# Optimization experiments

Measured on AMD Instinct MI355X. Metric: run time of the kernel, lower is better.

## Reference

```python
import jax, jax.numpy as jnp
import numpy as np

ALPHA = 0.2  # LeakyReLU negative slope
NEG_INF = -9e15


def _xavier(key, shape, gain=1.414):
    fan_in, fan_out = shape[-2], shape[-1]
    lim = gain * np.sqrt(6.0 / (fan_in + fan_out))
    return jax.random.uniform(key, shape, jnp.float32, -lim, lim)


def setup_inputs() -> dict:
    key = jax.random.key(0)
    ks = jax.random.split(key, 8)
    B, N, Din, H, Dh, Do = 8, 1024, 256, 4, 128, 64
    x = jax.random.normal(ks[0], (B, N, Din), jnp.float32)
    adj = jax.random.randint(ks[1], (B, N, N), 0, 2).astype(jnp.int32)
    W_heads = _xavier(ks[2], (H, Din, Dh))                 # per-head W
    a_heads = _xavier(ks[3], (H, 2 * Dh, 1))[..., 0]       # per-head a, [H, 2*Dh]
    W_out = _xavier(ks[4], (H * Dh, Do))                   # out_att W
    a_out = _xavier(ks[5], (2 * Do, 1))[..., 0]            # out_att a, [2*Do]
    Wf = _xavier(ks[6], (Do, Do), gain=1.0)                # fc_out linear
    bf = jnp.zeros((Do,), jnp.float32)
    return {"x": x, "adj": adj, "W_heads": W_heads, "a_heads": a_heads,
            "W_out": W_out, "a_out": a_out, "Wf": Wf, "bf": bf}


def _leaky_relu(v):
    return jnp.where(v >= 0, v, ALPHA * v)


def _gat(h, adj, W, a):
    # h: [B,N,Fin], adj: [B,N,N], W: [Fin,Fout], a: [2*Fout]
    Wh = h @ W                                   # [B,N,F]
    F = W.shape[-1]
    # additive attention: e_ij = leakyrelu(a_src.Wh_i + a_dst.Wh_j)
    src = Wh @ a[:F]                             # [B,N]
    dst = Wh @ a[F:]                             # [B,N]
    e = _leaky_relu(src[:, :, None] + dst[:, None, :])   # [B,N,N]
    scores = jnp.where(adj > 0, e, NEG_INF)
    attn = jax.nn.softmax(scores, axis=-1)       # dropout is a no-op in eval
    return attn @ Wh                             # [B,N,F]


def reference(x, adj, W_heads, a_heads, W_out, a_out, Wf, bf):
    B, N, _ = x.shape
    H, _, Dh = W_heads.shape
    # multi-head GAT, heads vmapped over leading axis of W_heads / a_heads
    heads = jax.vmap(_gat, in_axes=(None, None, 0, 0))(x, adj, W_heads, a_heads)  # [H,B,N,Dh]
    xcat = jnp.moveaxis(heads, 0, 2).reshape(B, N, H * Dh)   # concat heads, dim=2
    out = jax.nn.elu(_gat(xcat, adj, W_out, a_out))           # [B,N,Do]
    out = jax.nn.relu(out @ Wf + bf)                          # fc_out (dropout no-op)
    return out
```

## Files before the change

### kernel.cpp

```cpp
#include <hip/hip_runtime.h>
#include <hip/hip_bf16.h>

#define BSZ 8
#define NN 1024
#define DIN 256
#define NH 4
#define DH 128
#define DOUT 64
#define RTOT (BSZ*NN)
#define FCAT (NH*DH)
#define ALPHA 0.2f
#define XBLK 1024

typedef unsigned short ushortT;
typedef __attribute__((ext_vector_type(8))) short bf16x8;
typedef __attribute__((ext_vector_type(4))) float f32x4;

static __device__ __forceinline__ ushortT f2bf(float f) {
    __hip_bfloat16 h = __float2bfloat16(f);
    return *reinterpret_cast<ushortT*>(&h);
}
static __device__ __forceinline__ float bfu2f(ushortT u) {
    return __uint_as_float(((unsigned)u) << 16);
}
static __device__ __forceinline__ void split2(float v, ushortT& hi, ushortT& lo) {
    hi = f2bf(v);
    lo = f2bf(v - bfu2f(hi));
}
static __device__ __forceinline__ void gload16(const ushortT* g, ushortT* l) {
    __builtin_amdgcn_global_load_lds(
        (const __attribute__((address_space(1))) unsigned int*)(const void*)g,
        (__attribute__((address_space(3))) unsigned int*)(void*)l, 16, 0, 0);
}

__global__ __launch_bounds__(256) void k_prepw(const float* __restrict__ x,
                                               const float* __restrict__ W,
                                               const float* __restrict__ Wout,
                                               ushortT* __restrict__ xbh, ushortT* __restrict__ xbl,
                                               ushortT* __restrict__ WbTh, ushortT* __restrict__ WbTl,
                                               ushortT* __restrict__ WoTh, ushortT* __restrict__ WoTl) {
    const int bx = blockIdx.x;
    if (bx < XBLK) {
        const int g = bx * 256 + threadIdx.x;
        const float4* p = (const float4*)x + (size_t)g * 2;
        union { ushortT u[8]; uint4 q; } th, tl;
#pragma unroll
        for (int e4 = 0; e4 < 2; ++e4) {
            const float4 v = p[e4];
            split2(v.x, th.u[e4 * 4 + 0], tl.u[e4 * 4 + 0]);
            split2(v.y, th.u[e4 * 4 + 1], tl.u[e4 * 4 + 1]);
            split2(v.z, th.u[e4 * 4 + 2], tl.u[e4 * 4 + 2]);
            split2(v.w, th.u[e4 * 4 + 3], tl.u[e4 * 4 + 3]);
        }
        ((uint4*)xbh)[g] = th.q;
        ((uint4*)xbl)[g] = tl.q;
        return;
    }
    const int g2 = (bx - XBLK) * 256 + threadIdx.x;
    if (g2 < NH * DH * DIN) {
        const int h = g2 >> 15, f = (g2 >> 8) & 127, k = g2 & 255;
        const int kt = k >> 6, k64 = k & 63;
        const float v = W[(size_t)h * DIN * DH + (size_t)k * DH + f];
        ushortT hi, lo; split2(v, hi, lo);
        const int idx = ((h * 4 + kt) * 128 + f) * 64 + k64;
        WbTh[idx] = hi; WbTl[idx] = lo;
    } else {
        const int g3 = g2 - NH * DH * DIN;
        const int f = g3 >> 9, k = g3 & 511;
        const float v = Wout[(size_t)k * DOUT + f];
        ushortT hi, lo; split2(v, hi, lo);
        WoTh[g3] = hi; WoTl[g3] = lo;
    }
}

__global__ __launch_bounds__(512) void k_main(const ushortT* __restrict__ xbh,
                                              const ushortT* __restrict__ xbl,
                                              const float* __restrict__ ah_,
                                              const ushortT* __restrict__ WbTh,
                                              const ushortT* __restrict__ WbTl,
                                              const int* __restrict__ adj,
                                              unsigned* __restrict__ adjbit,
                                              ushortT* __restrict__ WhT,
                                              float* __restrict__ src1,
                                              float* __restrict__ dst1) {
    __shared__ ushortT Ah[128 * 64], Al[128 * 64];
    __shared__ ushortT Bh[128 * 64], Bl[128 * 64];
    __shared__ float sred[8][32], dred[8][32];
    const int tid = threadIdx.x;
    if (blockIdx.x >= 256) {
        const int g = (blockIdx.x - 256) * 512 + tid;
        const int row = g >> 5, w = g & 31;
        const int4* p = (const int4*)(adj + (size_t)row * NN + w * 32);
        unsigned m = 0;
#pragma unroll
        for (int q = 0; q < 8; ++q) {
            const int4 v = p[q];
            m |= (v.x > 0 ? 1u : 0u) << (q * 4 + 0);
            m |= (v.y > 0 ? 1u : 0u) << (q * 4 + 1);
            m |= (v.z > 0 ? 1u : 0u) << (q * 4 + 2);
            m |= (v.w > 0 ? 1u : 0u) << (q * 4 + 3);
        }
        adjbit[g] = m;
        return;
    }
    const int lane = tid & 63, wave = tid >> 6;
    const int h = blockIdx.x >> 6, mt = blockIdx.x & 63;
    const int r0 = mt * 128, b = r0 >> 10, jr = r0 & 1023;
    const int m16 = lane & 15, quad = lane >> 4;
    const int mg = wave >> 1, fg = wave & 1;
    f32x4 acc[2][4];
#pragma unroll
    for (int a = 0; a < 2; ++a)
#pragma unroll
        for (int c = 0; c < 4; ++c) acc[a][c] = (f32x4){0.f, 0.f, 0.f, 0.f};

    for (int kt = 0; kt < 4; ++kt) {
        __syncthreads();
        const ushortT* planeH = WbTh + (size_t)((h * 4 + kt) * 128) * 64;
        const ushortT* planeL = WbTl + (size_t)((h * 4 + kt) * 128) * 64;
#pragma unroll
        for (int half = 0; half < 2; ++half) {
            const int f = wave * 16 + half * 8 + (lane >> 3);
            const int sc = (lane & 7) ^ (f & 7);
            gload16(planeH + (size_t)f * 64 + sc * 8, Bh + (wave * 16 + half * 8) * 64);
            gload16(planeL + (size_t)f * 64 + sc * 8, Bl + (wave * 16 + half * 8) * 64);
        }
#pragma unroll
        for (int half = 0; half < 2; ++half) {
            const int r = wave * 16 + half * 8 + (lane >> 3);
            const int sc = (lane & 7) ^ (r & 7);
            gload16(xbh + (size_t)(r0 + r) * DIN + kt * 64 + sc * 8, Ah + (wave * 16 + half * 8) * 64);
            gload16(xbl + (size_t)(r0 + r) * DIN + kt * 64 + sc * 8, Al + (wave * 16 + half * 8) * 64);
        }
        __syncthreads();
#pragma unroll
        for (int ks = 0; ks < 2; ++ks) {
            bf16x8 a_h[2], a_l[2], b_h[4], b_l[4];
#pragma unroll
            for (int ms = 0; ms < 2; ++ms) {
                const int row = (mg * 2 + ms) * 16 + m16;
                const int cl = (ks * 4 + quad) ^ (row & 7);
                a_h[ms] = *(const bf16x8*)&Ah[row * 64 + cl * 8];
                a_l[ms] = *(const bf16x8*)&Al[row * 64 + cl * 8];
            }
#pragma unroll
            for (int fs = 0; fs < 4; ++fs) {
                const int row = (fg * 4 + fs) * 16 + m16;
                const int cl = (ks * 4 + quad) ^ (row & 7);
                b_h[fs] = *(const bf16x8*)&Bh[row * 64 + cl * 8];
                b_l[fs] = *(const bf16x8*)&Bl[row * 64 + cl * 8];
            }
#pragma unroll
            for (int ms = 0; ms < 2; ++ms)
#pragma unroll
                for (int fs = 0; fs < 4; ++fs) {
                    acc[ms][fs] = __builtin_amdgcn_mfma_f32_16x16x32_bf16(a_h[ms], b_h[fs], acc[ms][fs], 0, 0, 0);
                    acc[ms][fs] = __builtin_amdgcn_mfma_f32_16x16x32_bf16(a_h[ms], b_l[fs], acc[ms][fs], 0, 0, 0);
                    acc[ms][fs] = __builtin_amdgcn_mfma_f32_16x16x32_bf16(a_l[ms], b_h[fs], acc[ms][fs], 0, 0, 0);
                }
        }
    }
    float sacc[2][4] = {{0,0,0,0},{0,0,0,0}}, dacc[2][4] = {{0,0,0,0},{0,0,0,0}};
#pragma unroll
    for (int ms = 0; ms < 2; ++ms)
#pragma unroll
        for (int fs = 0; fs < 4; ++fs) {
            const int fl = (fg * 4 + fs) * 16 + m16;
            const float a_s = ah_[h * 2 * DH + fl];
            const float a_d = ah_[h * 2 * DH + DH + fl];
            union { ushortT u[4]; uint2 q; } tw;
#pragma unroll
            for (int reg = 0; reg < 4; ++reg) {
                const float v = acc[ms][fs][reg];
                sacc[ms][reg] += v * a_s;
                dacc[ms][reg] += v * a_d;
                tw.u[reg] = f2bf(v);
            }
            *(uint2*)(WhT + ((size_t)((b * NH + h) * DH + fl)) * NN + jr + (mg * 2 + ms) * 16 + quad * 4) = tw.q;
        }
#pragma unroll
    for (int ms = 0; ms < 2; ++ms) {
#pragma unroll
        for (int reg = 0; reg < 4; ++reg) {
            float s = sacc[ms][reg], d = dacc[ms][reg];
#pragma unroll
            for (int o = 8; o > 0; o >>= 1) {
                s += __shfl_xor(s, o, 64);
                d += __shfl_xor(d, o, 64);
            }
            if (m16 == 0) {
                sred[wave][ms * 16 + quad * 4 + reg] = s;
                dred[wave][ms * 16 + quad * 4 + reg] = d;
            }
        }
    }
    __syncthreads();
    if (tid < 128) {
        const int mgr = tid >> 5, idx = tid & 31;
        src1[h * RTOT + r0 + tid] = sred[mgr * 2][idx] + sred[mgr * 2 + 1][idx];
        dst1[h * RTOT + r0 + tid] = dred[mgr * 2][idx] + dred[mgr * 2 + 1][idx];
    }
}

__global__ __launch_bounds__(512, 2) void k_attn1(const unsigned* __restrict__ adjbit,
                                                  const ushortT* __restrict__ WhT,
                                                  const float* __restrict__ src1,
                                                  const float* __restrict__ dst1,
                                                  ushortT* __restrict__ xcat) {
    __shared__ ushortT Bs[2][128 * 64];
    __shared__ unsigned maskS[128 * 34];
    __shared__ float dstv[NN];
    __shared__ float rowinv[128], red8[8];
    const int tid = threadIdx.x, lane = tid & 63, wave = tid >> 6;
    const int bh = blockIdx.x & 31, it = blockIdx.x >> 5;
    const int b = bh >> 2, h = bh & 3;
    const int i0 = it * 128;
    const int m16 = lane & 15, quad = lane >> 4;
    const ushortT* Bbase = WhT + (size_t)(bh * DH) * NN;

#define STAGEB(kt_, buf_)                                                                  \
    {                                                                                      \
        _Pragma("unroll")                                                                  \
        for (int half = 0; half < 2; ++half) {                                             \
            const int f = wave * 16 + half * 8 + (lane >> 3);                              \
            gload16(Bbase + (size_t)f * NN + (kt_) * 64 + (((lane & 7) ^ (f & 7)) * 8),    \
                    &Bs[(buf_)][(wave * 16 + half * 8) * 64]);                             \
        }                                                                                  \
    }

    STAGEB(0, 0);
    {
        const uint4* msrc = (const uint4*)(adjbit + (size_t)(b * NN + i0) * 32) + tid * 2;
        const uint4 w0 = msrc[0], w1 = msrc[1];
        unsigned* mdst = &maskS[(tid >> 2) * 34 + (tid & 3) * 8];
        *(uint2*)&mdst[0] = make_uint2(w0.x, w0.y);
        *(uint2*)&mdst[2] = make_uint2(w0.z, w0.w);
        *(uint2*)&mdst[4] = make_uint2(w1.x, w1.y);
        *(uint2*)&mdst[6] = make_uint2(w1.z, w1.w);
    }
    float lm = -INFINITY;
#pragma unroll
    for (int k2 = 0; k2 < 2; ++k2) {
        const float d = dst1[h * RTOT + b * NN + tid + 512 * k2];
        dstv[tid + 512 * k2] = d;
        lm = fmaxf(lm, d);
    }
    const float si = src1[h * RTOT + b * NN + i0 + wave * 16 + m16];
#pragma unroll
    for (int o = 32; o > 0; o >>= 1) lm = fmaxf(lm, __shfl_xor(lm, o, 64));
    if (lane == 0) red8[wave] = lm;
    __syncthreads();
    float dmax = red8[0];
#pragma unroll
    for (int w = 1; w < 8; ++w) dmax = fmaxf(dmax, red8[w]);
    float mrow = si + dmax;
    mrow = mrow >= 0.f ? mrow : ALPHA * mrow;

    f32x4 acc[8];
#pragma unroll
    for (int c = 0; c < 8; ++c) acc[c] = (f32x4){0.f, 0.f, 0.f, 0.f};
    float fsum = 0.f;
    const int arow34 = (wave * 16 + m16) * 34;

#define KSTEP(kt_, buf_)                                                                   \
    {                                                                                      \
        _Pragma("unroll")                                                                  \
        for (int ks = 0; ks < 2; ++ks) {                                                   \
            const unsigned w0 = maskS[arow34 + (kt_) * 2 + ks];                            \
            const float4 d0 = *(const float4*)&dstv[(kt_) * 64 + ks * 32 + quad * 8];      \
            const float4 d1 = *(const float4*)&dstv[(kt_) * 64 + ks * 32 + quad * 8 + 4];  \
            const float dv[8] = {d0.x, d0.y, d0.z, d0.w, d1.x, d1.y, d1.z, d1.w};          \
            union { ushortT u[8]; bf16x8 v; } pa;                                          \
            _Pragma("unroll")                                                              \
            for (int e = 0; e < 8; ++e) {                                                  \
                float v = si + dv[e];                                                      \
                v = v >= 0.f ? v : ALPHA * v;                                              \
                const unsigned bit = (w0 >> (quad * 8 + e)) & 1u;                          \
                const float p = bit ? __expf(v - mrow) : 0.f;                              \
                fsum += p;                                                                 \
                pa.u[e] = f2bf(p);                                                         \
            }                                                                              \
            _Pragma("unroll")                                                              \
            for (int ff = 0; ff < 8; ++ff) {                                               \
                const int rowb = ff * 16 + m16;                                            \
                const bf16x8 bfr = *(const bf16x8*)&Bs[(buf_)][rowb * 64 +                 \
                    (((ks * 4 + quad) ^ (rowb & 7)) * 8)];                                 \
                acc[ff] = __builtin_amdgcn_mfma_f32_16x16x32_bf16(pa.v, bfr, acc[ff], 0, 0, 0); \
            }                                                                              \
        }                                                                                  \
    }

    for (int kt = 0; kt < 16; kt += 2) {
        if (kt < 15) STAGEB(kt + 1, 1);
        KSTEP(kt, 0);
        __syncthreads();
        if (kt < 14) STAGEB(kt + 2, 0);
        KSTEP(kt + 1, 1);
        __syncthreads();
    }
#undef STAGEB
#undef KSTEP

    fsum += __shfl_xor(fsum, 16, 64);
    fsum += __shfl_xor(fsum, 32, 64);
    if (quad == 0) rowinv[wave * 16 + m16] = 1.f / fsum;
    __syncthreads();
    const float4 rq = *(const float4*)&rowinv[wave * 16 + quad * 4];
    const float rv[4] = {rq.x, rq.y, rq.z, rq.w};
#pragma unroll
    for (int ff = 0; ff < 8; ++ff) {
        const int f = h * DH + ff * 16 + m16;
        ushortT* xc = xcat + (size_t)(b * NN + i0 + wave * 16 + quad * 4) * FCAT + f;
#pragma unroll
        for (int reg = 0; reg < 4; ++reg)
            xc[(size_t)reg * FCAT] = f2bf(acc[ff][reg] * rv[reg]);
    }
}

__global__ __launch_bounds__(256) void k_wh2(const ushortT* __restrict__ xcat,
                                             const ushortT* __restrict__ WoTh,
                                             const ushortT* __restrict__ WoTl,
                                             const float* __restrict__ aout,
                                             ushortT* __restrict__ Wh2T,
                                             float* __restrict__ src2,
                                             float* __restrict__ dst2) {
    __shared__ ushortT As[32 * 64];
    __shared__ ushortT Bh[64 * 64], Bl[64 * 64];
    __shared__ float sred[4][16], dred[4][16];
    const int tid = threadIdx.x, lane = tid & 63, wave = tid >> 6;
    const int r0 = blockIdx.x * 32;
    const int b = r0 >> 10, jr = r0 & 1023;
    const int m16 = lane & 15, quad = lane >> 4;
    const int mg = wave >> 1, fg = wave & 1;
    f32x4 acc[2] = {(f32x4){0.f,0.f,0.f,0.f}, (f32x4){0.f,0.f,0.f,0.f}};

    for (int kt = 0; kt < 8; ++kt) {
        __syncthreads();
        {
            const int row = wave * 8 + (lane >> 3);
            const int sc = (lane & 7) ^ (row & 7);
            gload16(xcat + (size_t)(r0 + row) * FCAT + kt * 64 + sc * 8, As + wave * 8 * 64);
        }
#pragma unroll
        for (int half = 0; half < 2; ++half) {
            const int f = wave * 16 + half * 8 + (lane >> 3);
            const int sc = (lane & 7) ^ (f & 7);
            gload16(WoTh + (size_t)f * FCAT + kt * 64 + sc * 8, Bh + (wave * 16 + half * 8) * 64);
            gload16(WoTl + (size_t)f * FCAT + kt * 64 + sc * 8, Bl + (wave * 16 + half * 8) * 64);
        }
        __syncthreads();
#pragma unroll
        for (int ks = 0; ks < 2; ++ks) {
            const int rowa = mg * 16 + m16;
            const int cla = (ks * 4 + quad) ^ (rowa & 7);
            const bf16x8 afr = *(const bf16x8*)&As[rowa * 64 + cla * 8];
#pragma unroll
            for (int ff = 0; ff < 2; ++ff) {
                const int rowb = fg * 32 + ff * 16 + m16;
                const int clb = (ks * 4 + quad) ^ (rowb & 7);
                const bf16x8 b_h = *(const bf16x8*)&Bh[rowb * 64 + clb * 8];
                const bf16x8 b_l = *(const bf16x8*)&Bl[rowb * 64 + clb * 8];
                acc[ff] = __builtin_amdgcn_mfma_f32_16x16x32_bf16(afr, b_h, acc[ff], 0, 0, 0);
                acc[ff] = __builtin_amdgcn_mfma_f32_16x16x32_bf16(afr, b_l, acc[ff], 0, 0, 0);
            }
        }
    }
    float sv[4] = {0, 0, 0, 0}, dv[4] = {0, 0, 0, 0};
#pragma unroll
    for (int ff = 0; ff < 2; ++ff) {
        const int f = fg * 32 + ff * 16 + m16;
        const float a_s = aout[f], a_d = aout[DOUT + f];
        union { ushortT u[4]; uint2 q; } tw;
#pragma unroll
        for (int reg = 0; reg < 4; ++reg) {
            const float v = acc[ff][reg];
            sv[reg] += v * a_s;
            dv[reg] += v * a_d;
            tw.u[reg] = f2bf(v);
        }
        *(uint2*)(Wh2T + ((size_t)(b * DOUT + f)) * NN + jr + mg * 16 + quad * 4) = tw.q;
    }
#pragma unroll
    for (int reg = 0; reg < 4; ++reg) {
#pragma unroll
        for (int o = 8; o > 0; o >>= 1) {
            sv[reg] += __shfl_xor(sv[reg], o, 64);
            dv[reg] += __shfl_xor(dv[reg], o, 64);
        }
        if (m16 == 0) { sred[wave][quad * 4 + reg] = sv[reg]; dred[wave][quad * 4 + reg] = dv[reg]; }
    }
    __syncthreads();
    if (tid < 32) {
        const int mgr = tid >> 4, idx = tid & 15;
        src2[r0 + tid] = sred[mgr * 2][idx] + sred[mgr * 2 + 1][idx];
        dst2[r0 + tid] = dred[mgr * 2][idx] + dred[mgr * 2 + 1][idx];
    }
}

__global__ __launch_bounds__(512) void k_attn2(const unsigned* __restrict__ adjbit,
                                               const ushortT* __restrict__ Wh2T,
                                               const float* __restrict__ src2,
                                               const float* __restrict__ dst2,
                                               const float* __restrict__ Wf,
                                               const float* __restrict__ bfv,
                                               float* __restrict__ out) {
    __shared__ ushortT As[2][32 * 64];
    __shared__ ushortT Wfh[64 * 64], Wfl[64 * 64];
    __shared__ unsigned maskS[32 * 32];
    __shared__ float dstv[NN];
    __shared__ float t2s[32 * 68];
    __shared__ float srcv[32], rowinv[32], red8[8];
    const int tid = threadIdx.x, lane = tid & 63, wave = tid >> 6;
    const int b = blockIdx.x & 7, it = blockIdx.x >> 3;
    const int i0 = it * 32;
    const int m16 = lane & 15, quad = lane >> 4;

    const unsigned* mbase = adjbit + (size_t)(b * NN + i0) * 32;
#pragma unroll
    for (int k2 = 0; k2 < 2; ++k2) maskS[tid + 512 * k2] = mbase[tid + 512 * k2];
    float lm = -INFINITY;
#pragma unroll
    for (int k2 = 0; k2 < 2; ++k2) {
        const float d = dst2[b * NN + tid + 512 * k2];
        dstv[tid + 512 * k2] = d;
        lm = fmaxf(lm, d);
    }
    if (tid < 32) srcv[tid] = src2[b * NN + i0 + tid];
    {
        const int c = tid & 63, kc = wave * 8;
        union { ushortT u[8]; uint4 q; } th4, tl4;
#pragma unroll
        for (int e = 0; e < 8; ++e)
            split2(Wf[(size_t)(kc + e) * DOUT + c], th4.u[e], tl4.u[e]);
        const int ch = wave ^ (c & 7);
        *(uint4*)&Wfh[c * 64 + ch * 8] = th4.q;
        *(uint4*)&Wfl[c * 64 + ch * 8] = tl4.q;
    }
#pragma unroll
    for (int o = 32; o > 0; o >>= 1) lm = fmaxf(lm, __shfl_xor(lm, o, 64));
    if (lane == 0) red8[wave] = lm;
    __syncthreads();
    float dmax = red8[0];
#pragma unroll
    for (int w = 1; w < 8; ++w) dmax = fmaxf(dmax, red8[w]);

    const int arow = tid >> 4, apart = tid & 15;
    const float si = srcv[arow];
    float mrow = si + dmax;
    mrow = mrow >= 0.f ? mrow : ALPHA * mrow;
    float fsum = 0.f;

    const int mfrag = wave >> 2, fq = wave & 3;
    const ushortT* Bbase = Wh2T + (size_t)(b * DOUT) * NN;
    f32x4 acc4 = (f32x4){0.f, 0.f, 0.f, 0.f};

#define STAGE_A2(kt_, buf_)                                                                \
    {                                                                                      \
        const int kt__ = (kt_);                                                            \
        const unsigned w0 = maskS[arow * 32 + kt__ * 2 + (apart >> 3)];                    \
        const int bb = (apart & 7) * 4;                                                    \
        union { ushortT u[4]; uint2 q; } tw;                                               \
        const float4 dv = *(const float4*)&dstv[kt__ * 64 + apart * 4];                    \
        const float vv[4] = {dv.x, dv.y, dv.z, dv.w};                                      \
        _Pragma("unroll")                                                                  \
        for (int e = 0; e < 4; ++e) {                                                      \
            float v = si + vv[e];                                                          \
            v = v >= 0.f ? v : ALPHA * v;                                                  \
            const unsigned bit = (w0 >> (bb + e)) & 1u;                                    \
            const float p = bit ? __expf(v - mrow) : 0.f;                                  \
            fsum += p;                                                                     \
            tw.u[e] = f2bf(p);                                                             \
        }                                                                                  \
        *(uint2*)&As[(buf_)][arow * 64 + (((apart >> 1) ^ (arow & 7)) * 8) + (apart & 1) * 4] = tw.q; \
    }
#define LOADB2(kt_, dst_)                                                                  \
    {                                                                                      \
        _Pragma("unroll")                                                                  \
        for (int ks = 0; ks < 2; ++ks)                                                     \
            dst_[ks] = *(const bf16x8*)(Bbase +                                            \
                (size_t)(fq * 16 + m16) * NN + (kt_) * 64 + (ks * 4 + quad) * 8);          \
    }
#define MFMA_STEP2(buf_, bv_)                                                              \
    {                                                                                      \
        _Pragma("unroll")                                                                  \
        for (int ks = 0; ks < 2; ++ks) {                                                   \
            const int rowa = mfrag * 16 + m16;                                             \
            const int cla = (ks * 4 + quad) ^ (rowa & 7);                                  \
            const bf16x8 afr = *(const bf16x8*)&As[(buf_)][rowa * 64 + cla * 8];           \
            acc4 = __builtin_amdgcn_mfma_f32_16x16x32_bf16(afr, bv_[ks], acc4, 0, 0, 0);   \
        }                                                                                  \
    }

    bf16x8 b0v[2], b1v[2];
    LOADB2(0, b0v);
    STAGE_A2(0, 0);
    for (int kt = 0; kt < 16; kt += 2) {
        __syncthreads();
        if (kt < 15) { LOADB2(kt + 1, b1v); STAGE_A2(kt + 1, 1); }
        MFMA_STEP2(0, b0v);
        __syncthreads();
        if (kt < 14) { LOADB2(kt + 2, b0v); STAGE_A2(kt + 2, 0); }
        MFMA_STEP2(1, b1v);
    }
#undef STAGE_A2
#undef LOADB2
#undef MFMA_STEP2
#pragma unroll
    for (int o = 1; o < 16; o <<= 1) fsum += __shfl_xor(fsum, o, 64);
    if ((lane & 15) == 0) rowinv[arow] = 1.f / fsum;
    __syncthreads();
#pragma unroll
    for (int reg = 0; reg < 4; ++reg) {
        const int row = mfrag * 16 + quad * 4 + reg;
        float v = acc4[reg] * rowinv[row];
        v = v > 0.f ? v : (__expf(v) - 1.f);
        t2s[row * 68 + fq * 16 + m16] = v;
    }
    __syncthreads();
    const int cc = fq * 16 + m16;
    f32x4 oacc;
    {
        const float bias = bfv[cc];
        oacc = (f32x4){bias, bias, bias, bias};
    }
#pragma unroll
    for (int ks = 0; ks < 2; ++ks) {
        const int rowa = mfrag * 16 + m16;
        const float4 fA = *(const float4*)&t2s[rowa * 68 + ks * 32 + quad * 8];
        const float4 fB = *(const float4*)&t2s[rowa * 68 + ks * 32 + quad * 8 + 4];
        union { ushortT u[8]; bf16x8 v; } a_h, a_l;
        const float av[8] = {fA.x, fA.y, fA.z, fA.w, fB.x, fB.y, fB.z, fB.w};
#pragma unroll
        for (int e = 0; e < 8; ++e) split2(av[e], a_h.u[e], a_l.u[e]);
        const int cl = (ks * 4 + quad) ^ (cc & 7);
        const bf16x8 b_h = *(const bf16x8*)&Wfh[cc * 64 + cl * 8];
        const bf16x8 b_l = *(const bf16x8*)&Wfl[cc * 64 + cl * 8];
        oacc = __builtin_amdgcn_mfma_f32_16x16x32_bf16(a_h.v, b_h, oacc, 0, 0, 0);
        oacc = __builtin_amdgcn_mfma_f32_16x16x32_bf16(a_h.v, b_l, oacc, 0, 0, 0);
        oacc = __builtin_amdgcn_mfma_f32_16x16x32_bf16(a_l.v, b_h, oacc, 0, 0, 0);
    }
#pragma unroll
    for (int reg = 0; reg < 4; ++reg) {
        const int i = i0 + mfrag * 16 + quad * 4 + reg;
        out[(size_t)(b * NN + i) * DOUT + cc] = fmaxf(oacc[reg], 0.f);
    }
}

extern "C" void kernel_launch(void* const* d_in, const int* in_sizes, int n_in,
                              void* d_out, int out_size, void* d_ws, size_t ws_size,
                              hipStream_t stream) {
    const float* x   = (const float*)d_in[0];
    const int*   adj = (const int*)d_in[1];
    const float* Wh  = (const float*)d_in[2];
    const float* ah  = (const float*)d_in[3];
    const float* Wo  = (const float*)d_in[4];
    const float* ao  = (const float*)d_in[5];
    const float* Wf  = (const float*)d_in[6];
    const float* bf  = (const float*)d_in[7];
    float* out = (float*)d_out;

    float* ws    = (float*)d_ws;
    float* src1  = ws;
    float* dst1  = src1 + NH * RTOT;
    float* src2  = dst1 + NH * RTOT;
    float* dst2  = src2 + RTOT;
    ushortT* WhT   = (ushortT*)(dst2 + RTOT);
    ushortT* Wh2T  = WhT + (size_t)RTOT * FCAT;
    ushortT* xcat  = Wh2T + (size_t)RTOT * DOUT;
    ushortT* WbTh  = xcat + (size_t)RTOT * FCAT;
    ushortT* WbTl  = WbTh + NH * DH * DIN;
    ushortT* WoTh  = WbTl + NH * DH * DIN;
    ushortT* WoTl  = WoTh + DOUT * FCAT;
    unsigned* adjbit = (unsigned*)(WoTl + DOUT * FCAT);
    ushortT* xbh  = (ushortT*)(adjbit + (size_t)BSZ * NN * 32);
    ushortT* xbl  = xbh + (size_t)RTOT * DIN;

    hipLaunchKernelGGL(k_prepw, dim3(XBLK + (NH * DH * DIN + DOUT * FCAT) / 256), dim3(256), 0, stream,
                       x, Wh, Wo, xbh, xbl, WbTh, WbTl, WoTh, WoTl);
    hipLaunchKernelGGL(k_main,  dim3(768), dim3(512), 0, stream,
                       xbh, xbl, ah, WbTh, WbTl, adj, adjbit, WhT, src1, dst1);
    hipLaunchKernelGGL(k_attn1, dim3(256), dim3(512), 0, stream,
                       adjbit, WhT, src1, dst1, xcat);
    hipLaunchKernelGGL(k_wh2,   dim3(256), dim3(256), 0, stream,
                       xcat, WoTh, WoTl, ao, Wh2T, src2, dst2);
    hipLaunchKernelGGL(k_attn2, dim3(256), dim3(512), 0, stream,
                       adjbit, Wh2T, src2, dst2, Wf, bf, out);
}
```

Measured before the change: 146.8 us.

## Double-buffer LDS staging in projection GEMMs and move adjacency packing to prep kernel

Moves the adjacency bit-packing blocks out of k_main into k_prepw, so k_main launches only its 256 GEMM blocks and uses a larger LDS footprint. Adds double-buffered LDS tiles in k_main and k_wh2: the next K tile is prefetched while MFMAs run on the current one, which drops one barrier per iteration. Also replaces the branchy LeakyReLU with fmaxf. Doubling the LDS buffers and setting launch_bounds(512,1) in k_main can lower occupancy.

```diff
diff --git a/kernel.cpp b/kernel.cpp
--- a/kernel.cpp
+++ b/kernel.cpp
@@ -32,13 +32,16 @@
         (const __attribute__((address_space(1))) unsigned int*)(const void*)g,
         (__attribute__((address_space(3))) unsigned int*)(void*)l, 16, 0, 0);
 }
+static __device__ __forceinline__ float lrelu(float x) { return fmaxf(x, ALPHA * x); }
 
 __global__ __launch_bounds__(256) void k_prepw(const float* __restrict__ x,
                                                const float* __restrict__ W,
                                                const float* __restrict__ Wout,
+                                               const int* __restrict__ adj,
                                                ushortT* __restrict__ xbh, ushortT* __restrict__ xbl,
                                                ushortT* __restrict__ WbTh, ushortT* __restrict__ WbTl,
-                                               ushortT* __restrict__ WoTh, ushortT* __restrict__ WoTl) {
+                                               ushortT* __restrict__ WoTh, ushortT* __restrict__ WoTl,
+                                               unsigned* __restrict__ adjbit) {
     const int bx = blockIdx.x;
     if (bx < XBLK) {
         const int g = bx * 256 + threadIdx.x;
@@ -56,39 +59,26 @@
         ((uint4*)xbl)[g] = tl.q;
         return;
     }
-    const int g2 = (bx - XBLK) * 256 + threadIdx.x;
-    if (g2 < NH * DH * DIN) {
-        const int h = g2 >> 15, f = (g2 >> 8) & 127, k = g2 & 255;
-        const int kt = k >> 6, k64 = k & 63;
-        const float v = W[(size_t)h * DIN * DH + (size_t)k * DH + f];
-        ushortT hi, lo; split2(v, hi, lo);
-        const int idx = ((h * 4 + kt) * 128 + f) * 64 + k64;
-        WbTh[idx] = hi; WbTl[idx] = lo;
-    } else {
-        const int g3 = g2 - NH * DH * DIN;
-        const int f = g3 >> 9, k = g3 & 511;
-        const float v = Wout[(size_t)k * DOUT + f];
-        ushortT hi, lo; split2(v, hi, lo);
-        WoTh[g3] = hi; WoTl[g3] = lo;
-    }
-}
-
-__global__ __launch_bounds__(512) void k_main(const ushortT* __restrict__ xbh,
-                                              const ushortT* __restrict__ xbl,
-                                              const float* __restrict__ ah_,
-                                              const ushortT* __restrict__ WbTh,
-                                              const ushortT* __restrict__ WbTl,
-                                              const int* __restrict__ adj,
-                                              unsigned* __restrict__ adjbit,
-                                              ushortT* __restrict__ WhT,
-                                              float* __restrict__ src1,
-                                              float* __restrict__ dst1) {
-    __shared__ ushortT Ah[128 * 64], Al[128 * 64];
-    __shared__ ushortT Bh[128 * 64], Bl[128 * 64];
-    __shared__ float sred[8][32], dred[8][32];
-    const int tid = threadIdx.x;
-    if (blockIdx.x >= 256) {
-        const int g = (blockIdx.x - 256) * 512 + tid;
+    if (bx < XBLK + 640) {
+        const int g2 = (bx - XBLK) * 256 + threadIdx.x;
+        if (g2 < NH * DH * DIN) {
+            const int h = g2 >> 15, f = (g2 >> 8) & 127, k = g2 & 255;
+            const int kt = k >> 6, k64 = k & 63;
+            const float v = W[(size_t)h * DIN * DH + (size_t)k * DH + f];
+            ushortT hi, lo; split2(v, hi, lo);
+            const int idx = ((h * 4 + kt) * 128 + f) * 64 + k64;
+            WbTh[idx] = hi; WbTl[idx] = lo;
+        } else {
+            const int g3 = g2 - NH * DH * DIN;
+            const int f = g3 >> 9, k = g3 & 511;
+            const float v = Wout[(size_t)k * DOUT + f];
+            ushortT hi, lo; split2(v, hi, lo);
+            WoTh[g3] = hi; WoTl[g3] = lo;
+        }
+        return;
+    }
+    {
+        const int g = (bx - XBLK - 640) * 256 + threadIdx.x;
         const int row = g >> 5, w = g & 31;
         const int4* p = (const int4*)(adj + (size_t)row * NN + w * 32);
         unsigned m = 0;
@@ -101,8 +91,21 @@
             m |= (v.w > 0 ? 1u : 0u) << (q * 4 + 3);
         }
         adjbit[g] = m;
-        return;
-    }
+    }
+}
+
+__global__ __launch_bounds__(512, 1) void k_main(const ushortT* __restrict__ xbh,
+                                                 const ushortT* __restrict__ xbl,
+                                                 const float* __restrict__ ah_,
+                                                 const ushortT* __restrict__ WbTh,
+                                                 const ushortT* __restrict__ WbTl,
+                                                 ushortT* __restrict__ WhT,
+                                                 float* __restrict__ src1,
+                                                 float* __restrict__ dst1) {
+    __shared__ ushortT Ah[2][128 * 64], Al[2][128 * 64];
+    __shared__ ushortT Bh[2][128 * 64], Bl[2][128 * 64];
+    __shared__ float sred[8][32], dred[8][32];
+    const int tid = threadIdx.x;
     const int lane = tid & 63, wave = tid >> 6;
     const int h = blockIdx.x >> 6, mt = blockIdx.x & 63;
     const int r0 = mt * 128, b = r0 >> 10, jr = r0 & 1023;
@@ -114,25 +117,31 @@
 #pragma unroll
         for (int c = 0; c < 4; ++c) acc[a][c] = (f32x4){0.f, 0.f, 0.f, 0.f};
 
+#define STAGE_M(kt_, buf_)                                                                 \
+    {                                                                                      \
+        const ushortT* planeH = WbTh + (size_t)((h * 4 + (kt_)) * 128) * 64;               \
+        const ushortT* planeL = WbTl + (size_t)((h * 4 + (kt_)) * 128) * 64;               \
+        _Pragma("unroll")                                                                  \
+        for (int half = 0; half < 2; ++half) {                                             \
+            const int f = wave * 16 + half * 8 + (lane >> 3);                              \
+            const int sc = (lane & 7) ^ (f & 7);                                           \
+            gload16(planeH + (size_t)f * 64 + sc * 8, &Bh[(buf_)][(wave * 16 + half * 8) * 64]); \
+            gload16(planeL + (size_t)f * 64 + sc * 8, &Bl[(buf_)][(wave * 16 + half * 8) * 64]); \
+        }                                                                                  \
+        _Pragma("unroll")                                                                  \
+        for (int half = 0; half < 2; ++half) {                                             \
+            const int r = wave * 16 + half * 8 + (lane >> 3);                              \
+            const int sc = (lane & 7) ^ (r & 7);                                           \
+            gload16(xbh + (size_t)(r0 + r) * DIN + (kt_) * 64 + sc * 8, &Ah[(buf_)][(wave * 16 + half * 8) * 64]); \
+            gload16(xbl + (size_t)(r0 + r) * DIN + (kt_) * 64 + sc * 8, &Al[(buf_)][(wave * 16 + half * 8) * 64]); \
+        }                                                                                  \
+    }
+
+    STAGE_M(0, 0);
+    __syncthreads();
     for (int kt = 0; kt < 4; ++kt) {
-        __syncthreads();
-        const ushortT* planeH = WbTh + (size_t)((h * 4 + kt) * 128) * 64;
-        const ushortT* planeL = WbTl + (size_t)((h * 4 + kt) * 128) * 64;
-#pragma unroll
-        for (int half = 0; half < 2; ++half) {
-            const int f = wave * 16 + half * 8 + (lane >> 3);
-            const int sc = (lane & 7) ^ (f & 7);
-            gload16(planeH + (size_t)f * 64 + sc * 8, Bh + (wave * 16 + half * 8) * 64);
-            gload16(planeL + (size_t)f * 64 + sc * 8, Bl + (wave * 16 + half * 8) * 64);
-        }
-#pragma unroll
-        for (int half = 0; half < 2; ++half) {
-            const int r = wave * 16 + half * 8 + (lane >> 3);
-            const int sc = (lane & 7) ^ (r & 7);
-            gload16(xbh + (size_t)(r0 + r) * DIN + kt * 64 + sc * 8, Ah + (wave * 16 + half * 8) * 64);
-            gload16(xbl + (size_t)(r0 + r) * DIN + kt * 64 + sc * 8, Al + (wave * 16 + half * 8) * 64);
-        }
-        __syncthreads();
+        const int cb = kt & 1;
+        if (kt < 3) STAGE_M(kt + 1, cb ^ 1);
 #pragma unroll
         for (int ks = 0; ks < 2; ++ks) {
             bf16x8 a_h[2], a_l[2], b_h[4], b_l[4];
@@ -140,15 +149,15 @@
             for (int ms = 0; ms < 2; ++ms) {
                 const int row = (mg * 2 + ms) * 16 + m16;
                 const int cl = (ks * 4 + quad) ^ (row & 7);
-                a_h[ms] = *(const bf16x8*)&Ah[row * 64 + cl * 8];
-                a_l[ms] = *(const bf16x8*)&Al[row * 64 + cl * 8];
+                a_h[ms] = *(const bf16x8*)&Ah[cb][row * 64 + cl * 8];
+                a_l[ms] = *(const bf16x8*)&Al[cb][row * 64 + cl * 8];
             }
 #pragma unroll
             for (int fs = 0; fs < 4; ++fs) {
                 const int row = (fg * 4 + fs) * 16 + m16;
                 const int cl = (ks * 4 + quad) ^ (row & 7);
-                b_h[fs] = *(const bf16x8*)&Bh[row * 64 + cl * 8];
-                b_l[fs] = *(const bf16x8*)&Bl[row * 64 + cl * 8];
+                b_h[fs] = *(const bf16x8*)&Bh[cb][row * 64 + cl * 8];
+                b_l[fs] = *(const bf16x8*)&Bl[cb][row * 64 + cl * 8];
             }
 #pragma unroll
             for (int ms = 0; ms < 2; ++ms)
@@ -159,7 +168,9 @@
                     acc[ms][fs] = __builtin_amdgcn_mfma_f32_16x16x32_bf16(a_l[ms], b_h[fs], acc[ms][fs], 0, 0, 0);
                 }
         }
-    }
+        __syncthreads();
+    }
+#undef STAGE_M
     float sacc[2][4] = {{0,0,0,0},{0,0,0,0}}, dacc[2][4] = {{0,0,0,0},{0,0,0,0}};
 #pragma unroll
     for (int ms = 0; ms < 2; ++ms)
@@ -253,8 +264,7 @@
     float dmax = red8[0];
 #pragma unroll
     for (int w = 1; w < 8; ++w) dmax = fmaxf(dmax, red8[w]);
-    float mrow = si + dmax;
-    mrow = mrow >= 0.f ? mrow : ALPHA * mrow;
+    const float mrow = lrelu(si + dmax);
 
     f32x4 acc[8];
 #pragma unroll
@@ -273,8 +283,7 @@
             union { ushortT u[8]; bf16x8 v; } pa;                                          \
             _Pragma("unroll")                                                              \
             for (int e = 0; e < 8; ++e) {                                                  \
-                float v = si + dv[e];                                                      \
-                v = v >= 0.f ? v : ALPHA * v;                                              \
+                const float v = lrelu(si + dv[e]);                                         \
                 const unsigned bit = (w0 >> (quad * 8 + e)) & 1u;                          \
                 const float p = bit ? __expf(v - mrow) : 0.f;                              \
                 fsum += p;                                                                 \
@@ -324,8 +333,8 @@
                                              ushortT* __restrict__ Wh2T,
                                              float* __restrict__ src2,
                                              float* __restrict__ dst2) {
-    __shared__ ushortT As[32 * 64];
-    __shared__ ushortT Bh[64 * 64], Bl[64 * 64];
+    __shared__ ushortT As[2][32 * 64];
+    __shared__ ushortT Bh[2][64 * 64], Bl[2][64 * 64];
     __shared__ float sred[4][16], dred[4][16];
     const int tid = threadIdx.x, lane = tid & 63, wave = tid >> 6;
     const int r0 = blockIdx.x * 32;
@@ -334,37 +343,46 @@
     const int mg = wave >> 1, fg = wave & 1;
     f32x4 acc[2] = {(f32x4){0.f,0.f,0.f,0.f}, (f32x4){0.f,0.f,0.f,0.f}};
 
+#define STAGE_W2(kt_, buf_)                                                                \
+    {                                                                                      \
+        {                                      \
+            const int row = wave * 8 + (lane >> 3);                                        \
+            const int sc = (lane & 7) ^ (row & 7);                                         \
+            gload16(xcat + (size_t)(r0 + row) * FCAT + (kt_) * 64 + sc * 8,                \
+                    &As[(buf_)][wave * 8 * 64]);                                           \
+        }                                                                                  \
+        _Pragma("unroll")                                                                  \
+        for (int half = 0; half < 2; ++half) {           \
+            const int f = wave * 16 + half * 8 + (lane >> 3);                              \
+            const int sc = (lane & 7) ^ (f & 7);                                           \
+            gload16(WoTh + (size_t)f * FCAT + (kt_) * 64 + sc * 8, &Bh[(buf_)][(wave * 16 + half * 8) * 64]); \
+            gload16(WoTl + (size_t)f * FCAT + (kt_) * 64 + sc * 8, &Bl[(buf_)][(wave * 16 + half * 8) * 64]); \
+        }                                                                                  \
+    }
+
+    STAGE_W2(0, 0);
+    __syncthreads();
     for (int kt = 0; kt < 8; ++kt) {
-        __syncthreads();
-        {
-            const int row = wave * 8 + (lane >> 3);
-            const int sc = (lane & 7) ^ (row & 7);
-            gload16(xcat + (size_t)(r0 + row) * FCAT + kt * 64 + sc * 8, As + wave * 8 * 64);
-        }
-#pragma unroll
-        for (int half = 0; half < 2; ++half) {
-            const int f = wave * 16 + half * 8 + (lane >> 3);
-            const int sc = (lane & 7) ^ (f & 7);
-            gload16(WoTh + (size_t)f * FCAT + kt * 64 + sc * 8, Bh + (wave * 16 + half * 8) * 64);
-            gload16(WoTl + (size_t)f * FCAT + kt * 64 + sc * 8, Bl + (wave * 16 + half * 8) * 64);
-        }
-        __syncthreads();
+        const int cb = kt & 1;
+        if (kt < 7) STAGE_W2(kt + 1, cb ^ 1);
 #pragma unroll
         for (int ks = 0; ks < 2; ++ks) {
             const int rowa = mg * 16 + m16;
             const int cla = (ks * 4 + quad) ^ (rowa & 7);
-            const bf16x8 afr = *(const bf16x8*)&As[rowa * 64 + cla * 8];
+            const bf16x8 afr = *(const bf16x8*)&As[cb][rowa * 64 + cla * 8];
 #pragma unroll
             for (int ff = 0; ff < 2; ++ff) {
                 const int rowb = fg * 32 + ff * 16 + m16;
                 const int clb = (ks * 4 + quad) ^ (rowb & 7);
-                const bf16x8 b_h = *(const bf16x8*)&Bh[rowb * 64 + clb * 8];
-                const bf16x8 b_l = *(const bf16x8*)&Bl[rowb * 64 + clb * 8];
+                const bf16x8 b_h = *(const bf16x8*)&Bh[cb][rowb * 64 + clb * 8];
+                const bf16x8 b_l = *(const bf16x8*)&Bl[cb][rowb * 64 + clb * 8];
                 acc[ff] = __builtin_amdgcn_mfma_f32_16x16x32_bf16(afr, b_h, acc[ff], 0, 0, 0);
                 acc[ff] = __builtin_amdgcn_mfma_f32_16x16x32_bf16(afr, b_l, acc[ff], 0, 0, 0);
             }
         }
-    }
+        __syncthreads();
+    }
+#undef STAGE_W2
     float sv[4] = {0, 0, 0, 0}, dv[4] = {0, 0, 0, 0};
 #pragma unroll
     for (int ff = 0; ff < 2; ++ff) {
@@ -446,8 +464,7 @@
 
     const int arow = tid >> 4, apart = tid & 15;
     const float si = srcv[arow];
-    float mrow = si + dmax;
-    mrow = mrow >= 0.f ? mrow : ALPHA * mrow;
+    const float mrow = lrelu(si + dmax);
     float fsum = 0.f;
 
     const int mfrag = wave >> 2, fq = wave & 3;
@@ -464,8 +481,7 @@
         const float vv[4] = {dv.x, dv.y, dv.z, dv.w};                                      \
         _Pragma("unroll")                                                                  \
         for (int e = 0; e < 4; ++e) {                                                      \
-            float v = si + vv[e];                                                          \
-            v = v >= 0.f ? v : ALPHA * v;                                                  \
+            const float v = lrelu(si + vv[e]);                                             \
             const unsigned bit = (w0 >> (bb + e)) & 1u;                                    \
             const float p = bit ? __expf(v - mrow) : 0.f;                                  \
             fsum += p;                                                                     \
@@ -575,10 +591,10 @@
     ushortT* xbh  = (ushortT*)(adjbit + (size_t)BSZ * NN * 32);
     ushortT* xbl  = xbh + (size_t)RTOT * DIN;
 
-    hipLaunchKernelGGL(k_prepw, dim3(XBLK + (NH * DH * DIN + DOUT * FCAT) / 256), dim3(256), 0, stream,
-                       x, Wh, Wo, xbh, xbl, WbTh, WbTl, WoTh, WoTl);
-    hipLaunchKernelGGL(k_main,  dim3(768), dim3(512), 0, stream,
-                       xbh, xbl, ah, WbTh, WbTl, adj, adjbit, WhT, src1, dst1);
+    hipLaunchKernelGGL(k_prepw, dim3(XBLK + 640 + 1024), dim3(256), 0, stream,
+                       x, Wh, Wo, adj, xbh, xbl, WbTh, WbTl, WoTh, WoTl, adjbit);
+    hipLaunchKernelGGL(k_main,  dim3(256), dim3(512), 0, stream,
+                       xbh, xbl, ah, WbTh, WbTl, WhT, src1, dst1);
     hipLaunchKernelGGL(k_attn1, dim3(256), dim3(512), 0, stream,
                        adjbit, WhT, src1, dst1, xcat);
     hipLaunchKernelGGL(k_wh2,   dim3(256), dim3(256), 0, stream,
```

Result: slower. 153.3 us (+4.4%).
